# Kernel tuning notes

Measured on AMD Instinct MI355X. Metric: run time of the kernel, lower is better.

## Reference

```python
import jax, jax.numpy as jnp
import numpy as np

L = 2048       # residues
NPAIR = 512    # inserted pair midpoints (unique i indices)
EP = 0.001
EPMAX = 40.0
EP_PAIR = 5.0
PAIR_LAMDA = 1.0


def _rigid_from_3points(x):
    # x: [N,3,3] -> rot [N,3,3], tran [N,3]
    x1, x2, x3 = x[:, 0], x[:, 1], x[:, 2]
    v1 = x3 - x2
    v2 = x1 - x2
    e1 = v1 / (jnp.linalg.norm(v1, axis=-1, keepdims=True) + 1e-3)
    u2 = v2 - e1 * jnp.sum(e1 * v2, axis=-1, keepdims=True)
    e2 = u2 / (jnp.linalg.norm(u2, axis=-1, keepdims=True) + 1e-8)
    e3 = jnp.cross(e1, e2)
    return jnp.stack([e1, e2, e3], axis=1), x2


def _fape_term(pred_flat, true_flat, p_rot, p_tran, t_rot, t_tran, ep, clamp):
    # pred_flat/true_flat: [P,3]; frames: [N,3,3]/[N,3]
    xp = jnp.einsum('npd,nkd->npk', pred_flat[None, :, :] - p_tran[:, None, :], p_rot)
    xt = jnp.einsum('npd,nkd->npk', true_flat[None, :, :] - t_tran[:, None, :], t_rot)
    dist = jnp.sqrt(jnp.sum((xp - xt) ** 2, axis=-1) + ep)  # [N,P]
    return jnp.mean(jnp.minimum(dist, clamp))


def _pair_indices(matrix):
    # replicate torch: nonzero, keep i<j, stable-sort by i (row-major order already is),
    # and the serial loop only ever inserts the FIRST pair for each i.
    m = np.asarray(matrix)
    m = np.triu(m, 1)
    ii, jj = np.nonzero(m)
    if ii.size == 0:
        return None, None
    keep = np.concatenate([[True], ii[1:] != ii[:-1]])
    return ii[keep], jj[keep]


def _concat_coords(coords, ii, jj):
    # vectorized version of concatenate_coordinates: insert midpoint of (i,j) after row i
    Lc = coords.shape[0]
    K = ii.shape[0]
    ins = (coords[ii] + coords[jj]) / 2
    orig_pos = np.arange(Lc) + np.searchsorted(ii, np.arange(Lc), side='left')
    ins_pos = ii + np.arange(K) + 1
    out = jnp.zeros((Lc + K,) + coords.shape[1:], coords.dtype)
    return out.at[orig_pos].set(coords).at[ins_pos].set(ins)


def setup_inputs() -> dict:
    key = jax.random.key(0)
    k1, k2 = jax.random.split(key)
    coor = jax.random.normal(k1, (L, 3, 3), dtype=jnp.float32) * 5.0
    target = coor + 0.5 * jax.random.normal(k2, (L, 3, 3), dtype=jnp.float32)
    p_rot, p_tran = _rigid_from_3points(coor)
    m = np.zeros((L, L), np.int32)
    i = np.arange(NPAIR) * 2          # unique i's, sorted
    m[i, i + L // 2] = 1              # i < j < L
    return {"coor": coor, "p_rot": p_rot, "p_tran": p_tran,
            "target": target, "matrix": jnp.asarray(m)}


def reference(coor, p_rot, p_tran, target, matrix):
    Lr = coor.shape[0]
    pred_flat = coor.reshape(Lr * 3, 3)
    true_flat = target.reshape(Lr * 3, 3)
    t_rot, t_tran = _rigid_from_3points(target)
    fape = _fape_term(pred_flat, true_flat, p_rot, p_tran, t_rot, t_tran, EP, EPMAX)

    ii, jj = _pair_indices(matrix)
    if ii is None:
        return fape / 10.0
    p_aug = _concat_coords(coor, ii, jj)
    t_aug = _concat_coords(target, ii, jj)
    p_rot_a, p_tran_a = _rigid_from_3points(p_aug)
    t_rot_a, t_tran_a = _rigid_from_3points(t_aug)
    fape_pair = _fape_term(pred_flat, true_flat, p_rot_a, p_tran_a, t_rot_a, t_tran_a, EP, EP_PAIR)
    return (fape + PAIR_LAMDA * fape_pair) / 10.0
```

## Files before the change

kernel.cpp:

```cpp
#include <hip/hip_runtime.h>
#include <math.h>
#include <limits.h>

#define LL 2048
#define PP (LL*3)
#define FPB 16
#define NP 8

__device__ int   g_firstj[LL];
__device__ int   g_cnt[LL];
__device__ int   g_ii[LL];
__device__ int   g_jj[LL];
__device__ int   g_K;
__device__ __align__(16) float g_frames[(3*LL)*12];
__device__ __align__(16) float g_pts[PP*8];
__device__ double g_sum[2];

__device__ inline void rigid3(const float* x, float* rot, float* tran) {
  float x1x=x[0],x1y=x[1],x1z=x[2];
  float x2x=x[3],x2y=x[4],x2z=x[5];
  float x3x=x[6],x3y=x[7],x3z=x[8];
  float v1x=x3x-x2x, v1y=x3y-x2y, v1z=x3z-x2z;
  float v2x=x1x-x2x, v2y=x1y-x2y, v2z=x1z-x2z;
  float n1 = sqrtf(v1x*v1x+v1y*v1y+v1z*v1z) + 0.001f;
  float e1x=v1x/n1, e1y=v1y/n1, e1z=v1z/n1;
  float dd = e1x*v2x+e1y*v2y+e1z*v2z;
  float u2x=v2x-e1x*dd, u2y=v2y-e1y*dd, u2z=v2z-e1z*dd;
  float n2 = sqrtf(u2x*u2x+u2y*u2y+u2z*u2z) + 1e-8f;
  float e2x=u2x/n2, e2y=u2y/n2, e2z=u2z/n2;
  rot[0]=e1x; rot[1]=e1y; rot[2]=e1z;
  rot[3]=e2x; rot[4]=e2y; rot[5]=e2z;
  rot[6]=e1y*e2z - e1z*e2y;
  rot[7]=e1z*e2x - e1x*e2z;
  rot[8]=e1x*e2y - e1y*e2x;
  tran[0]=x2x; tran[1]=x2y; tran[2]=x2z;
}

__device__ inline void packfr12(float* fr, const float* A, const float* tp,
                                const float* B, const float* tt) {
  float M[9];
  #pragma unroll
  for (int i = 0; i < 3; ++i)
    #pragma unroll
    for (int j = 0; j < 3; ++j)
      M[i*3+j] = A[0+i]*B[0+j] + A[3+i]*B[3+j] + A[6+i]*B[6+j];
  #pragma unroll
  for (int i = 0; i < 9; ++i) fr[i] = M[i];
  #pragma unroll
  for (int i = 0; i < 3; ++i)
    fr[9+i] = tp[i] - (M[i*3]*tt[0] + M[i*3+1]*tt[1] + M[i*3+2]*tt[2]);
}

__global__ void __launch_bounds__(256) k_prep(const int4* __restrict__ m4,
                                              const float* __restrict__ coor,
                                              const float* __restrict__ target,
                                              const float* __restrict__ prot,
                                              const float* __restrict__ ptran) {
  int bid = blockIdx.x;
  int t = threadIdx.x;
  if (bid < LL) {
    int i = bid;
    const int4* row = m4 + (size_t)i*512;
    int4 a = row[2*t], b = row[2*t+1];
    int j0 = t*8;
    int best = INT_MAX;
    if (a.x && (j0   > i)) best = j0;
    if (a.y && (j0+1 > i)) best = min(best, j0+1);
    if (a.z && (j0+2 > i)) best = min(best, j0+2);
    if (a.w && (j0+3 > i)) best = min(best, j0+3);
    if (b.x && (j0+4 > i)) best = min(best, j0+4);
    if (b.y && (j0+5 > i)) best = min(best, j0+5);
    if (b.z && (j0+6 > i)) best = min(best, j0+6);
    if (b.w && (j0+7 > i)) best = min(best, j0+7);
    for (int o = 32; o >= 1; o >>= 1) best = min(best, __shfl_xor(best, o));
    __shared__ int wmin[4];
    int lane = t & 63, wid = t >> 6;
    if (lane == 0) wmin[wid] = best;
    __syncthreads();
    if (t == 0)
      g_firstj[i] = min(min(wmin[0], wmin[1]), min(wmin[2], wmin[3]));
  } else if (bid < LL + 8) {
    int f = (bid - LL)*256 + t;
    if (f == 0) { g_sum[0] = 0.0; g_sum[1] = 0.0; }
    if (f >= LL) return;
    float B[9], tt[3];
    rigid3(target + f*9, B, tt);
    float A[9], tp[3];
    #pragma unroll
    for (int i = 0; i < 9; ++i) A[i] = prot[f*9+i];
    #pragma unroll
    for (int i = 0; i < 3; ++i) tp[i] = ptran[f*3+i];
    packfr12(g_frames + f*12, A, tp, B, tt);
  } else {
    int p = (bid - LL - 8)*256 + t;
    float4* o4 = reinterpret_cast<float4*>(g_pts);
    o4[p*2+0] = make_float4(coor[p*3], coor[p*3+1], coor[p*3+2], target[p*3]);
    o4[p*2+1] = make_float4(target[p*3+1], target[p*3+2], 0.f, 0.f);
  }
}

__global__ void __launch_bounds__(1024) k_scan() {
  int t = threadIdx.x;
  int r0 = 2*t, r1 = 2*t+1;
  int f0 = g_firstj[r0], f1 = g_firstj[r1];
  int h0 = (f0 != INT_MAX) ? 1 : 0;
  int h1 = (f1 != INT_MAX) ? 1 : 0;
  int local = h0 + h1;
  int lane = t & 63;
  int wid  = t >> 6;
  int incl = local;
  for (int o = 1; o < 64; o <<= 1) {
    int v = __shfl_up(incl, o);
    if (lane >= o) incl += v;
  }
  __shared__ int wsum[16];
  if (lane == 63) wsum[wid] = incl;
  __syncthreads();
  if (t < 16) {
    int iv = wsum[t];
    for (int o = 1; o < 16; o <<= 1) {
      int u = __shfl_up(iv, o);
      if (t >= o) iv += u;
    }
    wsum[t] = iv;
  }
  __syncthreads();
  int waveoff = (wid == 0) ? 0 : wsum[wid-1];
  int excl = waveoff + incl - local;
  g_cnt[r0] = excl;
  g_cnt[r1] = excl + h0;
  if (h0) { g_ii[excl]      = r0; g_jj[excl]      = f0; }
  if (h1) { g_ii[excl + h0] = r1; g_jj[excl + h0] = f1; }
  if (t == 1023) g_K = waveoff + incl;
}

__global__ void k_augfr(const float* __restrict__ coor,
                        const float* __restrict__ target) {
  int idx = blockIdx.x*blockDim.x + threadIdx.x;
  float xp[9], xt[9];
  int pos;
  if (idx < LL) {
    pos = idx + g_cnt[idx];
    #pragma unroll
    for (int c = 0; c < 9; ++c) { xp[c] = coor[idx*9+c]; xt[c] = target[idx*9+c]; }
  } else {
    int k = idx - LL;
    if (k >= g_K) return;
    int a = g_ii[k], b = g_jj[k];
    pos = a + k + 1;
    #pragma unroll
    for (int c = 0; c < 9; ++c) {
      xp[c] = 0.5f*(coor[a*9+c]   + coor[b*9+c]);
      xt[c] = 0.5f*(target[a*9+c] + target[b*9+c]);
    }
  }
  float A[9], tp[3], B[9], tt[3];
  rigid3(xp, A, tp);
  rigid3(xt, B, tt);
  packfr12(g_frames + (size_t)(LL + pos)*12, A, tp, B, tt);
}

__global__ void __launch_bounds__(256, 4) k_fape() {
  int Ftot = 2*LL + g_K;
  int f0 = blockIdx.y * FPB;
  if (f0 >= Ftot) return;
  int nf = min(FPB, Ftot - f0);
  int term1 = (f0 >= LL) ? 1 : 0;
  float clampv = term1 ? 5.f : 40.f;
  int t = threadIdx.x;

  int pbase = blockIdx.x*(256*NP) + t;
  const float4* pt4 = reinterpret_cast<const float4*>(g_pts);
  float px[NP], py[NP], pz[NP], ttx[NP], tty[NP], ttz[NP];
  #pragma unroll
  for (int k = 0; k < NP; ++k) {
    int p = pbase + k*256;
    float4 a = pt4[p*2+0];
    float4 b = pt4[p*2+1];
    px[k] = a.x; py[k] = a.y; pz[k] = a.z;
    ttx[k] = a.w; tty[k] = b.x; ttz[k] = b.y;
  }
  float acc = 0.f;

  const float4* fr4 = reinterpret_cast<const float4*>(g_frames) + (size_t)f0*3;
  #pragma unroll 2
  for (int q = 0; q < nf; ++q) {
    float4 w0 = fr4[q*3+0];
    float4 w1 = fr4[q*3+1];
    float4 w2 = fr4[q*3+2];
    #pragma unroll
    for (int k = 0; k < NP; ++k) {
      float m0 = fmaf(w0.x, ttx[k], fmaf(w0.y, tty[k], fmaf(w0.z, ttz[k], w2.y)));
      float m1 = fmaf(w0.w, ttx[k], fmaf(w1.x, tty[k], fmaf(w1.y, ttz[k], w2.z)));
      float m2 = fmaf(w1.z, ttx[k], fmaf(w1.w, tty[k], fmaf(w2.x, ttz[k], w2.w)));
      float dx = px[k] - m0, dy = py[k] - m1, dz = pz[k] - m2;
      float ss = fmaf(dx, dx, fmaf(dy, dy, fmaf(dz, dz, 0.001f)));
      acc += fminf(__builtin_amdgcn_sqrtf(ss), clampv);
    }
  }

  for (int o = 32; o >= 1; o >>= 1) acc += __shfl_down(acc, o);
  __shared__ float w[4];
  int lane = t & 63, wid = t >> 6;
  if (lane == 0) w[wid] = acc;
  __syncthreads();
  if (t == 0) {
    double s = (double)w[0] + (double)w[1] + (double)w[2] + (double)w[3];
    atomicAdd(&g_sum[term1], s);
  }
}

__global__ void k_final(float* __restrict__ out) {
  int K = g_K;
  double fape = g_sum[0] / ((double)LL * (double)PP);
  double r;
  if (K == 0) {
    r = fape / 10.0;
  } else {
    double fp = g_sum[1] / ((double)(LL + K) * (double)PP);
    r = (fape + fp) / 10.0;
  }
  out[0] = (float)r;
}

extern "C" void kernel_launch(void* const* d_in, const int* in_sizes, int n_in,
                              void* d_out, int out_size, void* d_ws, size_t ws_size,
                              hipStream_t stream) {
  const float* coor   = (const float*)d_in[0];
  const float* prot   = (const float*)d_in[1];
  const float* ptran  = (const float*)d_in[2];
  const float* target = (const float*)d_in[3];
  const int*   matrix = (const int*)d_in[4];
  float* out = (float*)d_out;

  k_prep<<<LL + 8 + PP/256, 256, 0, stream>>>((const int4*)matrix, coor, target, prot, ptran);
  k_scan<<<1, 1024, 0, stream>>>();
  k_augfr<<<16, 256, 0, stream>>>(coor, target);
  dim3 grid(PP/(256*NP), (3*LL)/FPB);
  k_fape<<<grid, 256, 0, stream>>>();
  k_final<<<1, 1, 0, stream>>>(out);
}
```

Measured before the change: 34.72 us.

## Fuse final reduction into FAPE kernel and stage frames in shared memory

Removes the separate single-thread finalize kernel by having the last FAPE block to finish, found through an atomic completion counter, compute the output. Each block now copies its frames into LDS once instead of every thread reading them from global memory. The launch bounds occupancy hint is dropped and the frame loop is no longer unrolled. This saves one kernel launch, but every block now does an extra atomic and a thread fence, and the second __syncthreads adds a little per-block overhead.

```diff
diff --git a/kernel.cpp b/kernel.cpp
--- a/kernel.cpp
+++ b/kernel.cpp
@@ -6,12 +6,14 @@
 #define PP (LL*3)
 #define FPB 16
 #define NP 8
+#define NBLK ((PP/(256*NP)) * ((3*LL)/FPB))
 
 __device__ int   g_firstj[LL];
 __device__ int   g_cnt[LL];
 __device__ int   g_ii[LL];
 __device__ int   g_jj[LL];
 __device__ int   g_K;
+__device__ int   g_done;
 __device__ __align__(16) float g_frames[(3*LL)*12];
 __device__ __align__(16) float g_pts[PP*8];
 __device__ double g_sum[2];
@@ -81,7 +83,7 @@
       g_firstj[i] = min(min(wmin[0], wmin[1]), min(wmin[2], wmin[3]));
   } else if (bid < LL + 8) {
     int f = (bid - LL)*256 + t;
-    if (f == 0) { g_sum[0] = 0.0; g_sum[1] = 0.0; }
+    if (f == 0) { g_sum[0] = 0.0; g_sum[1] = 0.0; g_done = 0; }
     if (f >= LL) return;
     float B[9], tt[3];
     rigid3(target + f*9, B, tt);
@@ -160,67 +162,75 @@
   packfr12(g_frames + (size_t)(LL + pos)*12, A, tp, B, tt);
 }
 
-__global__ void __launch_bounds__(256, 4) k_fape() {
+__global__ void __launch_bounds__(256) k_fape(float* __restrict__ out) {
+  __shared__ float4 shf[FPB*3];
   int Ftot = 2*LL + g_K;
   int f0 = blockIdx.y * FPB;
-  if (f0 >= Ftot) return;
-  int nf = min(FPB, Ftot - f0);
-  int term1 = (f0 >= LL) ? 1 : 0;
-  float clampv = term1 ? 5.f : 40.f;
   int t = threadIdx.x;
 
-  int pbase = blockIdx.x*(256*NP) + t;
-  const float4* pt4 = reinterpret_cast<const float4*>(g_pts);
-  float px[NP], py[NP], pz[NP], ttx[NP], tty[NP], ttz[NP];
-  #pragma unroll
-  for (int k = 0; k < NP; ++k) {
-    int p = pbase + k*256;
-    float4 a = pt4[p*2+0];
-    float4 b = pt4[p*2+1];
-    px[k] = a.x; py[k] = a.y; pz[k] = a.z;
-    ttx[k] = a.w; tty[k] = b.x; ttz[k] = b.y;
-  }
-  float acc = 0.f;
-
-  const float4* fr4 = reinterpret_cast<const float4*>(g_frames) + (size_t)f0*3;
-  #pragma unroll 2
-  for (int q = 0; q < nf; ++q) {
-    float4 w0 = fr4[q*3+0];
-    float4 w1 = fr4[q*3+1];
-    float4 w2 = fr4[q*3+2];
+  if (f0 < Ftot) {
+    int nf = min(FPB, Ftot - f0);
+    int term1 = (f0 >= LL) ? 1 : 0;
+    float clampv = term1 ? 5.f : 40.f;
+
+    const float4* gfr4 = reinterpret_cast<const float4*>(g_frames) + (size_t)f0*3;
+    if (t < nf*3) shf[t] = gfr4[t];
+    __syncthreads();
+
+    int pbase = blockIdx.x*(256*NP) + t;
+    const float4* pt4 = reinterpret_cast<const float4*>(g_pts);
+    float px[NP], py[NP], pz[NP], ttx[NP], tty[NP], ttz[NP];
     #pragma unroll
     for (int k = 0; k < NP; ++k) {
-      float m0 = fmaf(w0.x, ttx[k], fmaf(w0.y, tty[k], fmaf(w0.z, ttz[k], w2.y)));
-      float m1 = fmaf(w0.w, ttx[k], fmaf(w1.x, tty[k], fmaf(w1.y, ttz[k], w2.z)));
-      float m2 = fmaf(w1.z, ttx[k], fmaf(w1.w, tty[k], fmaf(w2.x, ttz[k], w2.w)));
-      float dx = px[k] - m0, dy = py[k] - m1, dz = pz[k] - m2;
-      float ss = fmaf(dx, dx, fmaf(dy, dy, fmaf(dz, dz, 0.001f)));
-      acc += fminf(__builtin_amdgcn_sqrtf(ss), clampv);
-    }
-  }
-
-  for (int o = 32; o >= 1; o >>= 1) acc += __shfl_down(acc, o);
-  __shared__ float w[4];
-  int lane = t & 63, wid = t >> 6;
-  if (lane == 0) w[wid] = acc;
-  __syncthreads();
+      int p = pbase + k*256;
+      float4 a = pt4[p*2+0];
+      float4 b = pt4[p*2+1];
+      px[k] = a.x; py[k] = a.y; pz[k] = a.z;
+      ttx[k] = a.w; tty[k] = b.x; ttz[k] = b.y;
+    }
+    float acc = 0.f;
+
+    #pragma unroll 1
+    for (int q = 0; q < nf; ++q) {
+      float4 w0 = shf[q*3+0];
+      float4 w1 = shf[q*3+1];
+      float4 w2 = shf[q*3+2];
+      #pragma unroll
+      for (int k = 0; k < NP; ++k) {
+        float m0 = fmaf(w0.x, ttx[k], fmaf(w0.y, tty[k], fmaf(w0.z, ttz[k], w2.y)));
+        float m1 = fmaf(w0.w, ttx[k], fmaf(w1.x, tty[k], fmaf(w1.y, ttz[k], w2.z)));
+        float m2 = fmaf(w1.z, ttx[k], fmaf(w1.w, tty[k], fmaf(w2.x, ttz[k], w2.w)));
+        float dx = px[k] - m0, dy = py[k] - m1, dz = pz[k] - m2;
+        float ss = fmaf(dx, dx, fmaf(dy, dy, fmaf(dz, dz, 0.001f)));
+        acc += fminf(__builtin_amdgcn_sqrtf(ss), clampv);
+      }
+    }
+
+    for (int o = 32; o >= 1; o >>= 1) acc += __shfl_down(acc, o);
+    __shared__ float w[4];
+    int lane = t & 63, wid = t >> 6;
+    if (lane == 0) w[wid] = acc;
+    __syncthreads();
+    if (t == 0) {
+      double s = (double)w[0] + (double)w[1] + (double)w[2] + (double)w[3];
+      atomicAdd(&g_sum[term1], s);
+    }
+  }
+
   if (t == 0) {
-    double s = (double)w[0] + (double)w[1] + (double)w[2] + (double)w[3];
-    atomicAdd(&g_sum[term1], s);
-  }
-}
-
-__global__ void k_final(float* __restrict__ out) {
-  int K = g_K;
-  double fape = g_sum[0] / ((double)LL * (double)PP);
-  double r;
-  if (K == 0) {
-    r = fape / 10.0;
-  } else {
-    double fp = g_sum[1] / ((double)(LL + K) * (double)PP);
-    r = (fape + fp) / 10.0;
-  }
-  out[0] = (float)r;
+    __threadfence();
+    int prev = atomicAdd(&g_done, 1);
+    if (prev == NBLK - 1) {
+      int K = g_K;
+      double s0 = atomicAdd(&g_sum[0], 0.0);
+      double s1 = atomicAdd(&g_sum[1], 0.0);
+      double fape = s0 / ((double)LL * (double)PP);
+      double r;
+      if (K == 0) r = fape / 10.0;
+      else        r = (fape + s1 / ((double)(LL + K) * (double)PP)) / 10.0;
+      out[0] = (float)r;
+    }
+  }
 }
 
 extern "C" void kernel_launch(void* const* d_in, const int* in_sizes, int n_in,
@@ -237,6 +247,5 @@
   k_scan<<<1, 1024, 0, stream>>>();
   k_augfr<<<16, 256, 0, stream>>>(coor, target);
   dim3 grid(PP/(256*NP), (3*LL)/FPB);
-  k_fape<<<grid, 256, 0, stream>>>();
-  k_final<<<1, 1, 0, stream>>>(out);
-}
+  k_fape<<<grid, 256, 0, stream>>>(out);
+}
```

After: 39.82 us. 14.7% more time.
